# Kernel tuning notes

Measured on AMD Instinct MI355X. Metric: run time of the kernel, lower is better.

Reference implementation:

```python
import math
import jax, jax.numpy as jnp
import numpy as np

N, T, F, H, C, P = 4096, 4, 256, 8, 16, 1024
D = F // H
RECONS_ERROR_LAMBDA = 0.1
L2_LAMBDA = 0.2
RECONS_LAMBDA = 0.01


def _xavier(key, shape):
    fan = shape[-1] + shape[-2]
    lim = math.sqrt(6.0 / fan)
    return jax.random.uniform(key, shape, minval=-lim, maxval=lim, dtype=jnp.float32)


def setup_inputs() -> dict:
    k = jax.random.split(jax.random.key(0), 12)
    return {
        "feature": jax.random.normal(k[0], (N, F), dtype=jnp.float32),
        "mask": (jax.random.uniform(k[1], (N, T, 1, N)) < 0.5).astype(jnp.float32),
        "node_multi_mask": jax.random.randint(k[2], (N,), 0, T),
        "node_idx": jax.random.randint(k[3], (P,), 0, N),
        "theta_w": _xavier(k[4], (F, F)),
        "theta_b": jnp.zeros((F,), jnp.float32),
        "linear": _xavier(k[5], (N, T, 1, N)),
        "recon_proj": _xavier(k[6], (T * T, F, F)),
        "mh_node_proj": _xavier(k[7], (T, F, F)),
        "mh_edge_proj": _xavier(k[8], (T * T, F, F)),
        "pred_w": _xavier(k[9], (C, F)),
        "pred_b": jnp.zeros((C,), jnp.float32),
    }


def reference(feature, mask, node_multi_mask, node_idx, theta_w, theta_b,
              linear, recon_proj, mh_node_proj, mh_edge_proj, pred_w, pred_b):
    nmm = node_multi_mask
    rows = jnp.arange(N)

    # theta linear
    feature = feature @ theta_w.T + theta_b  # [N,F]
    ff = jax.lax.stop_gradient(feature)      # feature.detach()

    # ---- HHEdgeCons ----
    linear_mask = linear * mask                              # [N,T,1,N]
    linear_selected = jnp.where(linear_mask > 0, linear_mask, 0.0)
    ls = linear_selected[:, :, 0, :]                         # [N,T,N]
    # matmul(linear_selected, inp_4_recon).squeeze(): each type t sees the same ff
    reconstruct = jnp.einsum('ntm,mf->ntf', ls, ff)          # [N,T,F]
    # node_project: out[i,j] = recon_proj[nmm[i]*T + j] @ ff[i]
    rp = recon_proj.reshape(T, T, F, F)
    proj_all = jnp.einsum('sjfg,ig->sijf', rp, ff)           # [T,N,T,F]
    inp_proj = proj_all[nmm, rows]                           # [N,T,F]
    l1 = jnp.sum(jnp.abs(ls))
    l2 = jnp.sum(jnp.sqrt(jnp.sum(ls * ls, axis=-1)))
    diff = inp_proj - reconstruct
    recon_error = jnp.sum(jnp.sqrt(jnp.sum(diff * diff, axis=-1)))
    recon_loss = RECONS_ERROR_LAMBDA * (RECONS_LAMBDA * recon_error + L2_LAMBDA * l2 + l1)

    # ---- HHEdgeMP ----
    edge_fea = jnp.einsum('ntm,mf->ntf', ls, feature) + feature[:, None, :]  # [N,T,F]
    edge_norm = jnp.sum(ls, axis=-1) + 1.0                   # [N,T]
    edge_fea = edge_fea / edge_norm[..., None]

    # ---- MultiheadWeight ----
    node_all = jnp.einsum('sfg,ng->snf', mh_node_proj, feature)  # [T,N,F]
    node_projd = node_all[nmm, rows]                             # [N,F]
    ep = mh_edge_proj.reshape(T, T, F, F)
    edge_all = jnp.einsum('sjfg,njg->snjf', ep, edge_fea)        # [T,N,T,F]
    edge_projd = edge_all[nmm, rows]                             # [N,T,F]
    node_multi = node_projd.reshape(N, 1, H, D).transpose(0, 2, 1, 3) / math.sqrt(D)  # [N,H,1,D]
    edge_multi = edge_projd.reshape(N, T, H, D).transpose(0, 2, 3, 1)                 # [N,H,D,T]
    scores = node_multi @ edge_multi                             # [N,H,1,T]
    # nn.Softmax(dim=1) -> over head axis
    all_r_weight = jax.nn.softmax(scores, axis=1).transpose(0, 3, 1, 2)  # [N,T,H,1]

    # ---- HHNodeMP (dropout = identity in eval) ----
    edge_mp = edge_fea.reshape(N, T, H, D)
    weighted = (all_r_weight * edge_mp).reshape(N, T, F)
    node_rep = jnp.sum(jax.nn.relu(weighted), axis=1)            # [N,F]

    # ---- Predictor (dropout = identity) ----
    logits = node_rep[node_idx] @ pred_w.T + pred_b              # [P,C]
    predict = jax.nn.softmax(jax.nn.sigmoid(logits), axis=1)
    return predict, recon_loss, node_rep
```

## Files before the change

kernel.cpp:

```cpp
#include <hip/hip_runtime.h>
#include <hip/hip_bf16.h>
#include <math.h>

#define NN 4096
#define NTROWS 16384

typedef __attribute__((ext_vector_type(8))) __bf16 bf16x8;
typedef __attribute__((ext_vector_type(4))) float f32x4;

static constexpr size_t OFF_SCAL   = 0;
static constexpr size_t OFF_CNT    = 64;
static constexpr size_t OFF_BASE   = 80;
static constexpr size_t OFF_PERM   = 256;
static constexpr size_t OFF_FEAT32 = 16896;
static constexpr size_t OFF_FEATB  = 4211200;
static constexpr size_t OFF_FEATPK = 6308352;
static constexpr size_t OFF_PACKS  = 8405504;
static constexpr size_t OFF_R      = 13255168;
static constexpr size_t OFF_EF32   = 30032384;
static constexpr size_t OFF_EFB    = 46809600;
static constexpr size_t OFF_NPROJ  = 55198208;
static constexpr size_t OFF_EPROJ  = 59392512;

__device__ __forceinline__ f32x4 mm_bf16(bf16x8 a, bf16x8 b, f32x4 c){
  return __builtin_amdgcn_mfma_f32_16x16x32_bf16(a, b, c, 0, 0, 0);
}

__global__ __launch_bounds__(256) void k1b_pack(
    const float* __restrict__ theta, const float* __restrict__ recp,
    const float* __restrict__ nodp,  const float* __restrict__ edgp,
    __bf16* __restrict__ packs)
{
  int b = blockIdx.x;
  const float* src;
  if (b == 0)       src = theta;
  else if (b < 17)  src = recp + (size_t)(b-1)*65536;
  else if (b < 21)  src = nodp + (size_t)(b-17)*65536;
  else              src = edgp + (size_t)(b-21)*65536;
  __bf16* dst = packs + (size_t)b*65536;
  for (int it = 0; it < 32; ++it){
    int u = it*256 + threadIdx.x;
    int lane = u & 63, cf = (u>>6)&15, ks = u>>10;
    int lo = lane & 15, hi = lane >> 4;
    const float* sp = src + (size_t)(cf*16+lo)*256 + ks*32 + hi*8;
    f32x4 a = *(const f32x4*)sp;
    f32x4 c = *(const f32x4*)(sp + 4);
    bf16x8 v;
    v[0]=(__bf16)a[0]; v[1]=(__bf16)a[1]; v[2]=(__bf16)a[2]; v[3]=(__bf16)a[3];
    v[4]=(__bf16)c[0]; v[5]=(__bf16)c[1]; v[6]=(__bf16)c[2]; v[7]=(__bf16)c[3];
    *(bf16x8*)(dst + (size_t)u*8) = v;
  }
}

__global__ __launch_bounds__(256) void k1c_pack(
    const float* __restrict__ feat32, __bf16* __restrict__ featPK)
{
  int u = blockIdx.x*256 + threadIdx.x;
  int lane = u & 63, cf = (u>>6)&15, ks = u>>10;
  int lo = lane & 15, hi = lane >> 4;
  const float* sp = feat32 + (size_t)(ks*32 + hi*8)*256 + cf*16 + lo;
  bf16x8 v;
#pragma unroll
  for (int i = 0; i < 8; ++i) v[i] = (__bf16)sp[(size_t)i*256];
  *(bf16x8*)(featPK + (size_t)u*8) = v;
}

__global__ __launch_bounds__(1024) void kbucket(
    const int* __restrict__ nmm, int* __restrict__ perm,
    int* __restrict__ counts, int* __restrict__ baseo)
{
  __shared__ int cl[4], bl[4], cur[4];
  int t = threadIdx.x;
  if (t < 4) cl[t] = 0;
  __syncthreads();
  for (int i = t; i < NN; i += 1024) atomicAdd(&cl[nmm[i]], 1);
  __syncthreads();
  if (t == 0){ int b = 0; for (int s = 0; s < 4; ++s){ bl[s] = b; b += cl[s]; } }
  __syncthreads();
  if (t < 4){ counts[t] = cl[t]; baseo[t] = bl[t]; cur[t] = bl[t]; }
  __syncthreads();
  for (int i = t; i < NN; i += 1024){
    int s = nmm[i];
    int p = atomicAdd(&cur[s], 1);
    perm[p] = i;
  }
}

template<int MODE>
__global__ __launch_bounds__(256) void gk(
    const __bf16* __restrict__ packs,
    const float*  __restrict__ featureA,
    const __bf16* __restrict__ featBA,
    const __bf16* __restrict__ efBA,
    const float*  __restrict__ tb,
    const float*  __restrict__ Rb,
    float* __restrict__ feat32o, __bf16* __restrict__ featBo,
    float* __restrict__ nprojo,  float* __restrict__ eprojo,
    float* __restrict__ scal,
    const int* __restrict__ perm, const int* __restrict__ counts,
    const int* __restrict__ baseo)
{
  __shared__ __align__(16) __bf16 Al[64*264];
  __shared__ int gidx[64];
  __shared__ float rowsq[64];
  const int t = threadIdx.x, lane = t & 63, wv = t >> 6;
  const int tile = blockIdx.x, combo = blockIdx.y;
  int s = 0, j = 0, cnt;
  const __bf16* B;
  const int rbase = tile * 64;
  if constexpr (MODE == 0){
    cnt = NN; B = packs;
  } else {
    if constexpr (MODE == 1){ s = combo; } else { s = combo >> 2; j = combo & 3; }
    cnt = counts[s];
    if (rbase >= cnt) return;
    int matb;
    if constexpr (MODE == 1)      matb = 17 + combo;
    else if constexpr (MODE == 2) matb = 1  + combo;
    else                          matb = 21 + combo;
    B = packs + (size_t)matb * 65536;
  }
  {
    int r = t >> 2, seg = t & 3;
    int g;
    if constexpr (MODE == 0) g = rbase + r;
    else { int pos = rbase + r; g = (pos < cnt) ? perm[baseo[s] + pos] : -1; }
    if (seg == 0) gidx[r] = g;
    if (t < 64) rowsq[t] = 0.f;
    __bf16* dstrow = &Al[r*264 + seg*64];
    if constexpr (MODE == 0){
      const float* srcp = featureA + (size_t)g*256 + seg*64;
#pragma unroll
      for (int q = 0; q < 8; ++q){
        f32x4 a = *(const f32x4*)(srcp + q*8);
        f32x4 c = *(const f32x4*)(srcp + q*8 + 4);
        bf16x8 v;
        v[0]=(__bf16)a[0]; v[1]=(__bf16)a[1]; v[2]=(__bf16)a[2]; v[3]=(__bf16)a[3];
        v[4]=(__bf16)c[0]; v[5]=(__bf16)c[1]; v[6]=(__bf16)c[2]; v[7]=(__bf16)c[3];
        *(bf16x8*)(dstrow + q*8) = v;
      }
    } else {
      const __bf16* srcp;
      if constexpr (MODE == 3) srcp = efBA + ((size_t)g*4 + j)*256 + seg*64;
      else                     srcp = featBA + (size_t)g*256 + seg*64;
      bf16x8 z;
#pragma unroll
      for (int i = 0; i < 8; ++i) z[i] = (__bf16)0.f;
#pragma unroll
      for (int q = 0; q < 8; ++q){
        bf16x8 v = (g >= 0) ? *(const bf16x8*)(srcp + q*8) : z;
        *(bf16x8*)(dstrow + q*8) = v;
      }
    }
  }
  __syncthreads();
  f32x4 acc[4][4];
#pragma unroll
  for (int a1 = 0; a1 < 4; ++a1)
#pragma unroll
    for (int a2 = 0; a2 < 4; ++a2){ f32x4 z = {0.f,0.f,0.f,0.f}; acc[a1][a2] = z; }
  const int m = lane & 15, h = lane >> 4;
#pragma unroll
  for (int ks = 0; ks < 8; ++ks){
    bf16x8 a[4];
#pragma unroll
    for (int rf = 0; rf < 4; ++rf)
      a[rf] = *(const bf16x8*)&Al[(rf*16 + m)*264 + ks*32 + h*8];
#pragma unroll
    for (int c4 = 0; c4 < 4; ++c4){
      int cf = wv*4 + c4;
      bf16x8 b = *(const bf16x8*)(B + ((size_t)(ks*16 + cf)*64 + lane)*8);
#pragma unroll
      for (int rf = 0; rf < 4; ++rf) acc[rf][c4] = mm_bf16(a[rf], b, acc[rf][c4]);
    }
  }
  if constexpr (MODE == 2){
#pragma unroll
    for (int rf = 0; rf < 4; ++rf)
#pragma unroll
      for (int reg = 0; reg < 4; ++reg){
        int row_l = rf*16 + h*4 + reg;
        int g2 = gidx[row_l];
        float sum = 0.f;
        if (g2 >= 0){
#pragma unroll
          for (int c4 = 0; c4 < 4; ++c4){
            int f = (wv*4 + c4)*16 + m;
            float d = acc[rf][c4][reg] - Rb[((size_t)g2*4 + j)*256 + f];
            sum += d*d;
          }
        }
        sum += __shfl_xor(sum, 1); sum += __shfl_xor(sum, 2);
        sum += __shfl_xor(sum, 4); sum += __shfl_xor(sum, 8);
        if (m == 0) atomicAdd(&rowsq[row_l], sum);
      }
    __syncthreads();
    if (t < 64){
      float e = sqrtf(rowsq[t]);
      e += __shfl_xor(e, 1);  e += __shfl_xor(e, 2);  e += __shfl_xor(e, 4);
      e += __shfl_xor(e, 8);  e += __shfl_xor(e, 16); e += __shfl_xor(e, 32);
      if (t == 0) atomicAdd(&scal[2], e);
    }
  } else {
#pragma unroll
    for (int rf = 0; rf < 4; ++rf)
#pragma unroll
      for (int c4 = 0; c4 < 4; ++c4){
        int f = (wv*4 + c4)*16 + m;
#pragma unroll
        for (int reg = 0; reg < 4; ++reg){
          int row_l = rf*16 + h*4 + reg;
          float val = acc[rf][c4][reg];
          if constexpr (MODE == 0){
            int n = rbase + row_l;
            float v2 = val + tb[f];
            feat32o[(size_t)n*256 + f] = v2;
            featBo[(size_t)n*256 + f] = (__bf16)v2;
          } else {
            int g2 = gidx[row_l];
            if (g2 >= 0){
              if constexpr (MODE == 1) nprojo[(size_t)g2*256 + f] = val;
              else eprojo[((size_t)g2*4 + j)*256 + f] = val;
            }
          }
        }
      }
  }
}

__global__ __launch_bounds__(512) void k2_main(
    const float* __restrict__ linear, const float* __restrict__ maskp,
    const __bf16* __restrict__ featPK, const float* __restrict__ feat32,
    float* __restrict__ Rb, float* __restrict__ ef32, __bf16* __restrict__ efB,
    float* __restrict__ scal)
{
  __shared__ __align__(16) __bf16 Al[64*72];
  __shared__ float ninv[64];
  const int t = threadIdx.x, lane = t & 63, wv = t >> 6;
  const int R0 = blockIdx.x * 64;
  const int r = t >> 3, ko = (t & 7) * 8;
  const float* lp = linear + (size_t)(R0 + r)*4096 + ko;
  const float* mp = maskp  + (size_t)(R0 + r)*4096 + ko;
  f32x4 l0 = *(const f32x4*)lp, l1r = *(const f32x4*)(lp + 4);
  f32x4 m0 = *(const f32x4*)mp, m1r = *(const f32x4*)(mp + 4);
  float rs = 0.f, rq = 0.f;
  f32x4 acc[4][2];
#pragma unroll
  for (int a1 = 0; a1 < 4; ++a1)
#pragma unroll
    for (int a2 = 0; a2 < 2; ++a2){ f32x4 z = {0.f,0.f,0.f,0.f}; acc[a1][a2] = z; }
  const int m = lane & 15, h = lane >> 4;

  for (int kc = 0; kc < 64; ++kc){
    __syncthreads();
    float v[8];
    v[0]=l0[0]*m0[0]; v[1]=l0[1]*m0[1]; v[2]=l0[2]*m0[2]; v[3]=l0[3]*m0[3];
    v[4]=l1r[0]*m1r[0]; v[5]=l1r[1]*m1r[1]; v[6]=l1r[2]*m1r[2]; v[7]=l1r[3]*m1r[3];
    bf16x8 pk;
#pragma unroll
    for (int i = 0; i < 8; ++i){
      float x = v[i] > 0.f ? v[i] : 0.f;
      rs += x; rq += x*x;
      pk[i] = (__bf16)x;
    }
    *(bf16x8*)&Al[r*72 + ko] = pk;
    if (kc < 63){
      lp += 64; mp += 64;
      l0 = *(const f32x4*)lp; l1r = *(const f32x4*)(lp + 4);
      m0 = *(const f32x4*)mp; m1r = *(const f32x4*)(mp + 4);
    }
    __syncthreads();
#pragma unroll
    for (int kl = 0; kl < 2; ++kl){
      bf16x8 a[4];
#pragma unroll
      for (int rf = 0; rf < 4; ++rf)
        a[rf] = *(const bf16x8*)&Al[(rf*16 + m)*72 + kl*32 + h*8];
#pragma unroll
      for (int ci = 0; ci < 2; ++ci){
        int cf = wv*2 + ci;
        bf16x8 b = *(const bf16x8*)(featPK + ((size_t)((kc*2 + kl)*16 + cf)*64 + lane)*8);
#pragma unroll
        for (int rf = 0; rf < 4; ++rf) acc[rf][ci] = mm_bf16(a[rf], b, acc[rf][ci]);
      }
    }
  }
  rs += __shfl_xor(rs, 1); rs += __shfl_xor(rs, 2); rs += __shfl_xor(rs, 4);
  rq += __shfl_xor(rq, 1); rq += __shfl_xor(rq, 2); rq += __shfl_xor(rq, 4);
  if ((t & 7) == 0) ninv[r] = 1.f/(rs + 1.f);
  float c1 = ((t & 7) == 0) ? rs : 0.f;
  float c2 = ((t & 7) == 0) ? sqrtf(rq) : 0.f;
#pragma unroll
  for (int msk = 1; msk < 64; msk <<= 1){
    c1 += __shfl_xor(c1, msk); c2 += __shfl_xor(c2, msk);
  }
  if (lane == 0){ atomicAdd(&scal[0], c1); atomicAdd(&scal[1], c2); }
  __syncthreads();
#pragma unroll
  for (int rf = 0; rf < 4; ++rf)
#pragma unroll
    for (int ci = 0; ci < 2; ++ci){
      int f = (wv*2 + ci)*16 + m;
#pragma unroll
      for (int reg = 0; reg < 4; ++reg){
        int row_l = rf*16 + h*4 + reg;
        float val = acc[rf][ci][reg];
        size_t gi = (size_t)(R0 + row_l)*256 + f;
        Rb[gi] = val;
        int n = (R0 + row_l) >> 2;
        float e = (val + feat32[(size_t)n*256 + f]) * ninv[row_l];
        ef32[gi] = e;
        efB[gi] = (__bf16)e;
      }
    }
}

__global__ __launch_bounds__(256) void k6_attn(
    const float* __restrict__ nproj, const float* __restrict__ eproj,
    const float* __restrict__ ef32, float* __restrict__ nrep)
{
  const int i = blockIdx.x, f = threadIdx.x, hh = f >> 5;
  __shared__ float sc[4][8];
  float np = nproj[(size_t)i*256 + f] * 0.17677669529663689f;
#pragma unroll
  for (int t4 = 0; t4 < 4; ++t4){
    float p = np * eproj[((size_t)i*4 + t4)*256 + f];
    p += __shfl_xor(p, 16); p += __shfl_xor(p, 8); p += __shfl_xor(p, 4);
    p += __shfl_xor(p, 2);  p += __shfl_xor(p, 1);
    if ((f & 31) == 0) sc[t4][hh] = p;
  }
  __syncthreads();
  float accv = 0.f;
#pragma unroll
  for (int t4 = 0; t4 < 4; ++t4){
    float mx = sc[t4][0];
#pragma unroll
    for (int q = 1; q < 8; ++q) mx = fmaxf(mx, sc[t4][q]);
    float den = 0.f;
#pragma unroll
    for (int q = 0; q < 8; ++q) den += expf(sc[t4][q] - mx);
    float w = expf(sc[t4][hh] - mx) / den;
    float x = w * ef32[((size_t)i*4 + t4)*256 + f];
    accv += x > 0.f ? x : 0.f;
  }
  nrep[(size_t)i*256 + f] = accv;
}

__global__ void k_loss(const float* __restrict__ scal, float* __restrict__ o){
  if (threadIdx.x == 0 && blockIdx.x == 0)
    o[0] = 0.1f*(0.01f*scal[2] + 0.2f*scal[1] + scal[0]);
}

__global__ __launch_bounds__(256) void k7_pred(
    const float* __restrict__ nrep, const int* __restrict__ nidx,
    const float* __restrict__ pw, const float* __restrict__ pb,
    float* __restrict__ outp)
{
  __shared__ float pwT[256*16];
  const int t = threadIdx.x;
  {
    int c0 = t & 15, k0 = (t >> 4) * 16;
    for (int kk = 0; kk < 16; ++kk)
      pwT[(k0 + kk)*16 + c0] = pw[(size_t)c0*256 + k0 + kk];
  }
  __syncthreads();
  const int c = t & 15, r0 = t >> 4;
  float pbv = pb[c];
  for (int rr = 0; rr < 4; ++rr){
    int p = blockIdx.x*64 + rr*16 + r0;
    int i = nidx[p];
    const float* nr = nrep + (size_t)i*256;
    float acc = pbv;
    for (int k = 0; k < 256; ++k) acc += nr[k]*pwT[k*16 + c];
    float sg = 1.f/(1.f + expf(-acc));
    float mx = sg;
    mx = fmaxf(mx, __shfl_xor(mx, 1)); mx = fmaxf(mx, __shfl_xor(mx, 2));
    mx = fmaxf(mx, __shfl_xor(mx, 4)); mx = fmaxf(mx, __shfl_xor(mx, 8));
    float ex = expf(sg - mx);
    float den = ex;
    den += __shfl_xor(den, 1); den += __shfl_xor(den, 2);
    den += __shfl_xor(den, 4); den += __shfl_xor(den, 8);
    outp[(size_t)p*16 + c] = ex/den;
  }
}

extern "C" void kernel_launch(void* const* d_in, const int* in_sizes, int n_in,
                              void* d_out, int out_size, void* d_ws, size_t ws_size,
                              hipStream_t stream)
{
  (void)in_sizes; (void)n_in; (void)out_size; (void)ws_size;
  const float* feature = (const float*)d_in[0];
  const float* maskp   = (const float*)d_in[1];
  const int*   nmm     = (const int*)d_in[2];
  const int*   nidx    = (const int*)d_in[3];
  const float* theta_w = (const float*)d_in[4];
  const float* theta_b = (const float*)d_in[5];
  const float* linear  = (const float*)d_in[6];
  const float* recon_p = (const float*)d_in[7];
  const float* node_p  = (const float*)d_in[8];
  const float* edge_p  = (const float*)d_in[9];
  const float* pred_w  = (const float*)d_in[10];
  const float* pred_b  = (const float*)d_in[11];
  float* out = (float*)d_out;
  char* ws = (char*)d_ws;

  float* scal   = (float*)(ws + OFF_SCAL);
  int*   counts = (int*)(ws + OFF_CNT);
  int*   baseo  = (int*)(ws + OFF_BASE);
  int*   perm   = (int*)(ws + OFF_PERM);
  float* feat32 = (float*)(ws + OFF_FEAT32);
  __bf16* featB  = (__bf16*)(ws + OFF_FEATB);
  __bf16* featPK = (__bf16*)(ws + OFF_FEATPK);
  __bf16* packs  = (__bf16*)(ws + OFF_PACKS);
  float* Rbuf   = (float*)(ws + OFF_R);
  float* ef32   = (float*)(ws + OFF_EF32);
  __bf16* efB    = (__bf16*)(ws + OFF_EFB);
  float* nproj  = (float*)(ws + OFF_NPROJ);
  float* eproj  = (float*)(ws + OFF_EPROJ);

  float* out_pred = out;
  float* out_loss = out + 16384;
  float* out_nrep = out + 16385;

  hipMemsetAsync(d_ws, 0, 96, stream);

  k1b_pack<<<37, 256, 0, stream>>>(theta_w, recon_p, node_p, edge_p, packs);

  gk<0><<<dim3(64, 1), 256, 0, stream>>>(packs, feature, nullptr, nullptr, theta_b,
      nullptr, feat32, featB, nullptr, nullptr, scal, perm, counts, baseo);

  k1c_pack<<<512, 256, 0, stream>>>(feat32, featPK);

  kbucket<<<1, 1024, 0, stream>>>(nmm, perm, counts, baseo);

  k2_main<<<256, 512, 0, stream>>>(linear, maskp, featPK, feat32,
                                   Rbuf, ef32, efB, scal);

  gk<2><<<dim3(64, 16), 256, 0, stream>>>(packs, nullptr, featB, nullptr, nullptr,
      Rbuf, nullptr, nullptr, nullptr, nullptr, scal, perm, counts, baseo);

  gk<3><<<dim3(64, 16), 256, 0, stream>>>(packs, nullptr, featB, efB, nullptr,
      nullptr, nullptr, nullptr, nullptr, eproj, scal, perm, counts, baseo);

  gk<1><<<dim3(64, 4), 256, 0, stream>>>(packs, nullptr, featB, nullptr, nullptr,
      nullptr, nullptr, nullptr, nproj, nullptr, scal, perm, counts, baseo);

  k6_attn<<<4096, 256, 0, stream>>>(nproj, eproj, ef32, out_nrep);

  k_loss<<<1, 64, 0, stream>>>(scal, out_loss);

  k7_pred<<<16, 256, 0, stream>>>(out_nrep, nidx, pred_w, pred_b, out_pred);
}
```

Measured before the change: 847.1 us.

## Split-K the masked reconstruction GEMM and merge projection GEMMs into one launch

The main masked-linear GEMM (k2_main) now splits its K=4096 reduction across 4 blocks per row tile, using a double-buffered LDS tile. Partial results are accumulated with atomics into a zeroed R buffer, and per-row sum and sum-of-squares are also accumulated with atomics. A new k2b kernel then does the normalization, builds the edge features and reduces the losses. The three projection GEMM launches are fused into a single gk_all grid. kbucket is rewritten to use wave ballots instead of shared atomics and is launched first. The aim is to fill more CUs with the memory-bound 256-block GEMM and cut launch count, at the cost of a 17MB memset, float atomics (nondeterministic summation order) and an extra pass over R.

```diff
diff --git a/kernel.cpp b/kernel.cpp
--- a/kernel.cpp
+++ b/kernel.cpp
@@ -17,10 +17,12 @@
 static constexpr size_t OFF_FEATPK = 6308352;
 static constexpr size_t OFF_PACKS  = 8405504;
 static constexpr size_t OFF_R      = 13255168;
-static constexpr size_t OFF_EF32   = 30032384;
-static constexpr size_t OFF_EFB    = 46809600;
-static constexpr size_t OFF_NPROJ  = 55198208;
-static constexpr size_t OFF_EPROJ  = 59392512;
+static constexpr size_t OFF_RSUM   = 30032384;
+static constexpr size_t OFF_RSQ    = 30097920;
+static constexpr size_t OFF_EF32   = 30163456;
+static constexpr size_t OFF_EFB    = 46940672;
+static constexpr size_t OFF_NPROJ  = 55329280;
+static constexpr size_t OFF_EPROJ  = 59523584;
 
 __device__ __forceinline__ f32x4 mm_bf16(bf16x8 a, bf16x8 b, f32x4 c){
   return __builtin_amdgcn_mfma_f32_16x16x32_bf16(a, b, c, 0, 0, 0);
@@ -69,88 +71,70 @@
     const int* __restrict__ nmm, int* __restrict__ perm,
     int* __restrict__ counts, int* __restrict__ baseo)
 {
-  __shared__ int cl[4], bl[4], cur[4];
-  int t = threadIdx.x;
-  if (t < 4) cl[t] = 0;
-  __syncthreads();
-  for (int i = t; i < NN; i += 1024) atomicAdd(&cl[nmm[i]], 1);
-  __syncthreads();
-  if (t == 0){ int b = 0; for (int s = 0; s < 4; ++s){ bl[s] = b; b += cl[s]; } }
-  __syncthreads();
-  if (t < 4){ counts[t] = cl[t]; baseo[t] = bl[t]; cur[t] = bl[t]; }
-  __syncthreads();
-  for (int i = t; i < NN; i += 1024){
+  __shared__ int segoff[64][4];
+  __shared__ int bl[4];
+  const int t = threadIdx.x, lane = t & 63, w = t >> 6;
+  int sv[4];
+#pragma unroll
+  for (int it = 0; it < 4; ++it){
+    int i = it*1024 + t;
     int s = nmm[i];
-    int p = atomicAdd(&cur[s], 1);
-    perm[p] = i;
-  }
-}
-
-template<int MODE>
-__global__ __launch_bounds__(256) void gk(
-    const __bf16* __restrict__ packs,
-    const float*  __restrict__ featureA,
-    const __bf16* __restrict__ featBA,
-    const __bf16* __restrict__ efBA,
-    const float*  __restrict__ tb,
-    const float*  __restrict__ Rb,
-    float* __restrict__ feat32o, __bf16* __restrict__ featBo,
-    float* __restrict__ nprojo,  float* __restrict__ eprojo,
-    float* __restrict__ scal,
-    const int* __restrict__ perm, const int* __restrict__ counts,
-    const int* __restrict__ baseo)
+    sv[it] = s;
+#pragma unroll
+    for (int b = 0; b < 4; ++b){
+      unsigned long long mb = __ballot(s == b);
+      if (lane == 0) segoff[it*16 + w][b] = __popcll(mb);
+    }
+  }
+  __syncthreads();
+  if (t < 4){
+    int b = t, run = 0;
+    for (int seg = 0; seg < 64; ++seg){
+      int c = segoff[seg][b]; segoff[seg][b] = run; run += c;
+    }
+    counts[b] = run;
+  }
+  __syncthreads();
+  if (t == 0){
+    int b0 = 0;
+    for (int s = 0; s < 4; ++s){ bl[s] = b0; baseo[s] = b0; b0 += counts[s]; }
+  }
+  __syncthreads();
+#pragma unroll
+  for (int it = 0; it < 4; ++it){
+    int i = it*1024 + t;
+    int s = sv[it];
+    int rank = 0;
+#pragma unroll
+    for (int b = 0; b < 4; ++b){
+      unsigned long long mb = __ballot(s == b);
+      if (s == b) rank = __popcll(mb & ((1ull << lane) - 1ull));
+    }
+    perm[bl[s] + segoff[it*16 + w][s] + rank] = i;
+  }
+}
+
+__global__ __launch_bounds__(256) void k0_feat(
+    const __bf16* __restrict__ packs, const float* __restrict__ featureA,
+    const float* __restrict__ tb,
+    float* __restrict__ feat32o, __bf16* __restrict__ featBo)
 {
   __shared__ __align__(16) __bf16 Al[64*264];
-  __shared__ int gidx[64];
-  __shared__ float rowsq[64];
   const int t = threadIdx.x, lane = t & 63, wv = t >> 6;
-  const int tile = blockIdx.x, combo = blockIdx.y;
-  int s = 0, j = 0, cnt;
-  const __bf16* B;
-  const int rbase = tile * 64;
-  if constexpr (MODE == 0){
-    cnt = NN; B = packs;
-  } else {
-    if constexpr (MODE == 1){ s = combo; } else { s = combo >> 2; j = combo & 3; }
-    cnt = counts[s];
-    if (rbase >= cnt) return;
-    int matb;
-    if constexpr (MODE == 1)      matb = 17 + combo;
-    else if constexpr (MODE == 2) matb = 1  + combo;
-    else                          matb = 21 + combo;
-    B = packs + (size_t)matb * 65536;
-  }
+  const int rbase = blockIdx.x * 64;
+  const __bf16* B = packs;
   {
     int r = t >> 2, seg = t & 3;
-    int g;
-    if constexpr (MODE == 0) g = rbase + r;
-    else { int pos = rbase + r; g = (pos < cnt) ? perm[baseo[s] + pos] : -1; }
-    if (seg == 0) gidx[r] = g;
-    if (t < 64) rowsq[t] = 0.f;
+    const float* srcp = featureA + (size_t)(rbase + r)*256 + seg*64;
     __bf16* dstrow = &Al[r*264 + seg*64];
-    if constexpr (MODE == 0){
-      const float* srcp = featureA + (size_t)g*256 + seg*64;
-#pragma unroll
-      for (int q = 0; q < 8; ++q){
-        f32x4 a = *(const f32x4*)(srcp + q*8);
-        f32x4 c = *(const f32x4*)(srcp + q*8 + 4);
-        bf16x8 v;
-        v[0]=(__bf16)a[0]; v[1]=(__bf16)a[1]; v[2]=(__bf16)a[2]; v[3]=(__bf16)a[3];
-        v[4]=(__bf16)c[0]; v[5]=(__bf16)c[1]; v[6]=(__bf16)c[2]; v[7]=(__bf16)c[3];
-        *(bf16x8*)(dstrow + q*8) = v;
-      }
-    } else {
-      const __bf16* srcp;
-      if constexpr (MODE == 3) srcp = efBA + ((size_t)g*4 + j)*256 + seg*64;
-      else                     srcp = featBA + (size_t)g*256 + seg*64;
-      bf16x8 z;
-#pragma unroll
-      for (int i = 0; i < 8; ++i) z[i] = (__bf16)0.f;
-#pragma unroll
-      for (int q = 0; q < 8; ++q){
-        bf16x8 v = (g >= 0) ? *(const bf16x8*)(srcp + q*8) : z;
-        *(bf16x8*)(dstrow + q*8) = v;
-      }
+#pragma unroll
+    for (int q = 0; q < 8; ++q){
+      f32x4 a = *(const f32x4*)(srcp + q*8);
+      f32x4 c = *(const f32x4*)(srcp + q*8 + 4);
+      bf16x8 v;
+      v[0]=(__bf16)a[0]; v[1]=(__bf16)a[1]; v[2]=(__bf16)a[2]; v[3]=(__bf16)a[3];
+      v[4]=(__bf16)c[0]; v[5]=(__bf16)c[1]; v[6]=(__bf16)c[2]; v[7]=(__bf16)c[3];
+      *(bf16x8*)(dstrow + q*8) = v;
     }
   }
   __syncthreads();
@@ -174,7 +158,184 @@
       for (int rf = 0; rf < 4; ++rf) acc[rf][c4] = mm_bf16(a[rf], b, acc[rf][c4]);
     }
   }
-  if constexpr (MODE == 2){
+#pragma unroll
+  for (int rf = 0; rf < 4; ++rf)
+#pragma unroll
+    for (int c4 = 0; c4 < 4; ++c4){
+      int f = (wv*4 + c4)*16 + m;
+#pragma unroll
+      for (int reg = 0; reg < 4; ++reg){
+        int n = rbase + rf*16 + h*4 + reg;
+        float v2 = acc[rf][c4][reg] + tb[f];
+        feat32o[(size_t)n*256 + f] = v2;
+        featBo[(size_t)n*256 + f] = (__bf16)v2;
+      }
+    }
+}
+
+__global__ __launch_bounds__(512, 4) void k2_main(
+    const float* __restrict__ linear, const float* __restrict__ maskp,
+    const __bf16* __restrict__ featPK,
+    float* __restrict__ Rb, float* __restrict__ rowsum, float* __restrict__ rowsq)
+{
+  __shared__ __align__(16) __bf16 Al[2][64*72];
+  const int t = threadIdx.x, lane = t & 63, wv = t >> 6;
+  const int R0 = blockIdx.x * 64;
+  const int ksl = blockIdx.y;
+  const int r = t >> 3, ko = (t & 7) * 8;
+  const float* lp = linear + (size_t)(R0 + r)*4096 + ksl*1024 + ko;
+  const float* mp = maskp  + (size_t)(R0 + r)*4096 + ksl*1024 + ko;
+  const __bf16* Bp = featPK + (((size_t)(ksl*32)*16 + wv*2)*64 + lane)*8;
+  f32x4 l0 = *(const f32x4*)lp, l1r = *(const f32x4*)(lp + 4);
+  f32x4 m0 = *(const f32x4*)mp, m1r = *(const f32x4*)(mp + 4);
+  float rs = 0.f, rq = 0.f;
+  f32x4 acc[4][2];
+#pragma unroll
+  for (int a1 = 0; a1 < 4; ++a1)
+#pragma unroll
+    for (int a2 = 0; a2 < 2; ++a2){ f32x4 z = {0.f,0.f,0.f,0.f}; acc[a1][a2] = z; }
+  const int m = lane & 15, h = lane >> 4;
+
+  for (int kc = 0; kc < 16; ++kc){
+    bf16x8 b[2][2];
+#pragma unroll
+    for (int kl = 0; kl < 2; ++kl)
+#pragma unroll
+      for (int ci = 0; ci < 2; ++ci)
+        b[kl][ci] = *(const bf16x8*)(Bp + (size_t)(kc*2 + kl)*8192 + ci*512);
+    __builtin_amdgcn_sched_barrier(0);
+    float v[8];
+    v[0]=l0[0]*m0[0]; v[1]=l0[1]*m0[1]; v[2]=l0[2]*m0[2]; v[3]=l0[3]*m0[3];
+    v[4]=l1r[0]*m1r[0]; v[5]=l1r[1]*m1r[1]; v[6]=l1r[2]*m1r[2]; v[7]=l1r[3]*m1r[3];
+    bf16x8 pk;
+#pragma unroll
+    for (int i = 0; i < 8; ++i){
+      float x = v[i] > 0.f ? v[i] : 0.f;
+      rs += x; rq += x*x;
+      pk[i] = (__bf16)x;
+    }
+    *(bf16x8*)&Al[kc & 1][r*72 + ko] = pk;
+    if (kc < 15){
+      lp += 64; mp += 64;
+      l0 = *(const f32x4*)lp; l1r = *(const f32x4*)(lp + 4);
+      m0 = *(const f32x4*)mp; m1r = *(const f32x4*)(mp + 4);
+    }
+    __builtin_amdgcn_sched_barrier(0);
+    __syncthreads();
+#pragma unroll
+    for (int kl = 0; kl < 2; ++kl){
+      bf16x8 a[4];
+#pragma unroll
+      for (int rf = 0; rf < 4; ++rf)
+        a[rf] = *(const bf16x8*)&Al[kc & 1][(rf*16 + m)*72 + kl*32 + h*8];
+#pragma unroll
+      for (int ci = 0; ci < 2; ++ci)
+#pragma unroll
+        for (int rf = 0; rf < 4; ++rf) acc[rf][ci] = mm_bf16(a[rf], b[kl][ci], acc[rf][ci]);
+    }
+  }
+  rs += __shfl_xor(rs, 1); rs += __shfl_xor(rs, 2); rs += __shfl_xor(rs, 4);
+  rq += __shfl_xor(rq, 1); rq += __shfl_xor(rq, 2); rq += __shfl_xor(rq, 4);
+  if ((t & 7) == 0){
+    atomicAdd(&rowsum[R0 + r], rs);
+    atomicAdd(&rowsq[R0 + r], rq);
+  }
+#pragma unroll
+  for (int rf = 0; rf < 4; ++rf)
+#pragma unroll
+    for (int ci = 0; ci < 2; ++ci){
+      int f = (wv*2 + ci)*16 + m;
+#pragma unroll
+      for (int reg = 0; reg < 4; ++reg){
+        int row_l = rf*16 + h*4 + reg;
+        atomicAdd(&Rb[(size_t)(R0 + row_l)*256 + f], acc[rf][ci][reg]);
+      }
+    }
+}
+
+__global__ __launch_bounds__(256) void k2b(
+    const float* __restrict__ Rb, const float* __restrict__ feat32,
+    const float* __restrict__ rowsum, const float* __restrict__ rowsq,
+    float* __restrict__ ef32, __bf16* __restrict__ efB, float* __restrict__ scal)
+{
+  const int t = threadIdx.x;
+  const int row0 = blockIdx.x * 16;
+#pragma unroll 4
+  for (int rr = 0; rr < 16; ++rr){
+    int row = row0 + rr, n = row >> 2;
+    float ninv = 1.f / (rowsum[row] + 1.f);
+    size_t gi = (size_t)row*256 + t;
+    float e = (Rb[gi] + feat32[(size_t)n*256 + t]) * ninv;
+    ef32[gi] = e;
+    efB[gi] = (__bf16)e;
+  }
+  float c1 = 0.f, c2 = 0.f;
+  if (t < 16){ int row = row0 + t; c1 = rowsum[row]; c2 = sqrtf(rowsq[row]); }
+  c1 += __shfl_xor(c1, 1); c1 += __shfl_xor(c1, 2); c1 += __shfl_xor(c1, 4); c1 += __shfl_xor(c1, 8);
+  c2 += __shfl_xor(c2, 1); c2 += __shfl_xor(c2, 2); c2 += __shfl_xor(c2, 4); c2 += __shfl_xor(c2, 8);
+  if (t == 0){ atomicAdd(&scal[0], c1); atomicAdd(&scal[1], c2); }
+}
+
+__global__ __launch_bounds__(256) void gk_all(
+    const __bf16* __restrict__ packs, const __bf16* __restrict__ featB,
+    const __bf16* __restrict__ efB, const float* __restrict__ Rb,
+    float* __restrict__ nproj, float* __restrict__ eproj, float* __restrict__ scal,
+    const int* __restrict__ perm, const int* __restrict__ counts,
+    const int* __restrict__ baseo)
+{
+  __shared__ __align__(16) __bf16 Al[64*264];
+  __shared__ int gidx[64];
+  __shared__ float rowsq_l[64];
+  const int t = threadIdx.x, lane = t & 63, wv = t >> 6;
+  const int y = blockIdx.y;
+  int mode, s, j, matb;
+  if (y < 16){ mode = 2; s = y >> 2; j = y & 3; matb = 1 + y; }
+  else if (y < 32){ int y2 = y - 16; mode = 3; s = y2 >> 2; j = y2 & 3; matb = 21 + y2; }
+  else { mode = 1; s = y - 32; j = 0; matb = 17 + s; }
+  const int cnt = counts[s];
+  const int rbase = blockIdx.x * 64;
+  if (rbase >= cnt) return;
+  const __bf16* B = packs + (size_t)matb * 65536;
+  {
+    int r = t >> 2, seg = t & 3;
+    int pos = rbase + r;
+    int g = (pos < cnt) ? perm[baseo[s] + pos] : -1;
+    if (seg == 0) gidx[r] = g;
+    if (t < 64) rowsq_l[t] = 0.f;
+    const __bf16* srcp = (mode == 3) ? efB + ((size_t)g*4 + j)*256 + seg*64
+                                     : featB + (size_t)g*256 + seg*64;
+    __bf16* dstrow = &Al[r*264 + seg*64];
+    bf16x8 z;
+#pragma unroll
+    for (int i = 0; i < 8; ++i) z[i] = (__bf16)0.f;
+#pragma unroll
+    for (int q = 0; q < 8; ++q){
+      bf16x8 v = (g >= 0) ? *(const bf16x8*)(srcp + q*8) : z;
+      *(bf16x8*)(dstrow + q*8) = v;
+    }
+  }
+  __syncthreads();
+  f32x4 acc[4][4];
+#pragma unroll
+  for (int a1 = 0; a1 < 4; ++a1)
+#pragma unroll
+    for (int a2 = 0; a2 < 4; ++a2){ f32x4 z = {0.f,0.f,0.f,0.f}; acc[a1][a2] = z; }
+  const int m = lane & 15, h = lane >> 4;
+#pragma unroll
+  for (int ks = 0; ks < 8; ++ks){
+    bf16x8 a[4];
+#pragma unroll
+    for (int rf = 0; rf < 4; ++rf)
+      a[rf] = *(const bf16x8*)&Al[(rf*16 + m)*264 + ks*32 + h*8];
+#pragma unroll
+    for (int c4 = 0; c4 < 4; ++c4){
+      int cf = wv*4 + c4;
+      bf16x8 b = *(const bf16x8*)(B + ((size_t)(ks*16 + cf)*64 + lane)*8);
+#pragma unroll
+      for (int rf = 0; rf < 4; ++rf) acc[rf][c4] = mm_bf16(a[rf], b, acc[rf][c4]);
+    }
+  }
+  if (mode == 2){
 #pragma unroll
     for (int rf = 0; rf < 4; ++rf)
 #pragma unroll
@@ -192,11 +353,11 @@
         }
         sum += __shfl_xor(sum, 1); sum += __shfl_xor(sum, 2);
         sum += __shfl_xor(sum, 4); sum += __shfl_xor(sum, 8);
-        if (m == 0) atomicAdd(&rowsq[row_l], sum);
+        if (m == 0) atomicAdd(&rowsq_l[row_l], sum);
       }
     __syncthreads();
     if (t < 64){
-      float e = sqrtf(rowsq[t]);
+      float e = sqrtf(rowsq_l[t]);
       e += __shfl_xor(e, 1);  e += __shfl_xor(e, 2);  e += __shfl_xor(e, 4);
       e += __shfl_xor(e, 8);  e += __shfl_xor(e, 16); e += __shfl_xor(e, 32);
       if (t == 0) atomicAdd(&scal[2], e);
@@ -210,109 +371,14 @@
 #pragma unroll
         for (int reg = 0; reg < 4; ++reg){
           int row_l = rf*16 + h*4 + reg;
-          float val = acc[rf][c4][reg];
-          if constexpr (MODE == 0){
-            int n = rbase + row_l;
-            float v2 = val + tb[f];
-            feat32o[(size_t)n*256 + f] = v2;
-            featBo[(size_t)n*256 + f] = (__bf16)v2;
-          } else {
-            int g2 = gidx[row_l];
-            if (g2 >= 0){
-              if constexpr (MODE == 1) nprojo[(size_t)g2*256 + f] = val;
-              else eprojo[((size_t)g2*4 + j)*256 + f] = val;
-            }
+          int g2 = gidx[row_l];
+          if (g2 >= 0){
+            if (mode == 1) nproj[(size_t)g2*256 + f] = acc[rf][c4][reg];
+            else           eproj[((size_t)g2*4 + j)*256 + f] = acc[rf][c4][reg];
           }
         }
       }
   }
-}
-
-__global__ __launch_bounds__(512) void k2_main(
-    const float* __restrict__ linear, const float* __restrict__ maskp,
-    const __bf16* __restrict__ featPK, const float* __restrict__ feat32,
-    float* __restrict__ Rb, float* __restrict__ ef32, __bf16* __restrict__ efB,
-    float* __restrict__ scal)
-{
-  __shared__ __align__(16) __bf16 Al[64*72];
-  __shared__ float ninv[64];
-  const int t = threadIdx.x, lane = t & 63, wv = t >> 6;
-  const int R0 = blockIdx.x * 64;
-  const int r = t >> 3, ko = (t & 7) * 8;
-  const float* lp = linear + (size_t)(R0 + r)*4096 + ko;
-  const float* mp = maskp  + (size_t)(R0 + r)*4096 + ko;
-  f32x4 l0 = *(const f32x4*)lp, l1r = *(const f32x4*)(lp + 4);
-  f32x4 m0 = *(const f32x4*)mp, m1r = *(const f32x4*)(mp + 4);
-  float rs = 0.f, rq = 0.f;
-  f32x4 acc[4][2];
-#pragma unroll
-  for (int a1 = 0; a1 < 4; ++a1)
-#pragma unroll
-    for (int a2 = 0; a2 < 2; ++a2){ f32x4 z = {0.f,0.f,0.f,0.f}; acc[a1][a2] = z; }
-  const int m = lane & 15, h = lane >> 4;
-
-  for (int kc = 0; kc < 64; ++kc){
-    __syncthreads();
-    float v[8];
-    v[0]=l0[0]*m0[0]; v[1]=l0[1]*m0[1]; v[2]=l0[2]*m0[2]; v[3]=l0[3]*m0[3];
-    v[4]=l1r[0]*m1r[0]; v[5]=l1r[1]*m1r[1]; v[6]=l1r[2]*m1r[2]; v[7]=l1r[3]*m1r[3];
-    bf16x8 pk;
-#pragma unroll
-    for (int i = 0; i < 8; ++i){
-      float x = v[i] > 0.f ? v[i] : 0.f;
-      rs += x; rq += x*x;
-      pk[i] = (__bf16)x;
-    }
-    *(bf16x8*)&Al[r*72 + ko] = pk;
-    if (kc < 63){
-      lp += 64; mp += 64;
-      l0 = *(const f32x4*)lp; l1r = *(const f32x4*)(lp + 4);
-      m0 = *(const f32x4*)mp; m1r = *(const f32x4*)(mp + 4);
-    }
-    __syncthreads();
-#pragma unroll
-    for (int kl = 0; kl < 2; ++kl){
-      bf16x8 a[4];
-#pragma unroll
-      for (int rf = 0; rf < 4; ++rf)
-        a[rf] = *(const bf16x8*)&Al[(rf*16 + m)*72 + kl*32 + h*8];
-#pragma unroll
-      for (int ci = 0; ci < 2; ++ci){
-        int cf = wv*2 + ci;
-        bf16x8 b = *(const bf16x8*)(featPK + ((size_t)((kc*2 + kl)*16 + cf)*64 + lane)*8);
-#pragma unroll
-        for (int rf = 0; rf < 4; ++rf) acc[rf][ci] = mm_bf16(a[rf], b, acc[rf][ci]);
-      }
-    }
-  }
-  rs += __shfl_xor(rs, 1); rs += __shfl_xor(rs, 2); rs += __shfl_xor(rs, 4);
-  rq += __shfl_xor(rq, 1); rq += __shfl_xor(rq, 2); rq += __shfl_xor(rq, 4);
-  if ((t & 7) == 0) ninv[r] = 1.f/(rs + 1.f);
-  float c1 = ((t & 7) == 0) ? rs : 0.f;
-  float c2 = ((t & 7) == 0) ? sqrtf(rq) : 0.f;
-#pragma unroll
-  for (int msk = 1; msk < 64; msk <<= 1){
-    c1 += __shfl_xor(c1, msk); c2 += __shfl_xor(c2, msk);
-  }
-  if (lane == 0){ atomicAdd(&scal[0], c1); atomicAdd(&scal[1], c2); }
-  __syncthreads();
-#pragma unroll
-  for (int rf = 0; rf < 4; ++rf)
-#pragma unroll
-    for (int ci = 0; ci < 2; ++ci){
-      int f = (wv*2 + ci)*16 + m;
-#pragma unroll
-      for (int reg = 0; reg < 4; ++reg){
-        int row_l = rf*16 + h*4 + reg;
-        float val = acc[rf][ci][reg];
-        size_t gi = (size_t)(R0 + row_l)*256 + f;
-        Rb[gi] = val;
-        int n = (R0 + row_l) >> 2;
-        float e = (val + feat32[(size_t)n*256 + f]) * ninv[row_l];
-        ef32[gi] = e;
-        efB[gi] = (__bf16)e;
-      }
-    }
 }
 
 __global__ __launch_bounds__(256) void k6_attn(
@@ -413,6 +479,8 @@
   __bf16* featPK = (__bf16*)(ws + OFF_FEATPK);
   __bf16* packs  = (__bf16*)(ws + OFF_PACKS);
   float* Rbuf   = (float*)(ws + OFF_R);
+  float* rowsum = (float*)(ws + OFF_RSUM);
+  float* rowsq  = (float*)(ws + OFF_RSQ);
   float* ef32   = (float*)(ws + OFF_EF32);
   __bf16* efB    = (__bf16*)(ws + OFF_EFB);
   float* nproj  = (float*)(ws + OFF_NPROJ);
@@ -422,28 +490,24 @@
   float* out_loss = out + 16384;
   float* out_nrep = out + 16385;
 
-  hipMemsetAsync(d_ws, 0, 96, stream);
+  hipMemsetAsync(ws + OFF_SCAL, 0, 96, stream);
+  hipMemsetAsync(ws + OFF_R, 0, 16777216 + 131072, stream);
+
+  kbucket<<<1, 1024, 0, stream>>>(nmm, perm, counts, baseo);
 
   k1b_pack<<<37, 256, 0, stream>>>(theta_w, recon_p, node_p, edge_p, packs);
 
-  gk<0><<<dim3(64, 1), 256, 0, stream>>>(packs, feature, nullptr, nullptr, theta_b,
-      nullptr, feat32, featB, nullptr, nullptr, scal, perm, counts, baseo);
+  k0_feat<<<64, 256, 0, stream>>>(packs, feature, theta_b, feat32, featB);
 
   k1c_pack<<<512, 256, 0, stream>>>(feat32, featPK);
 
-  kbucket<<<1, 1024, 0, stream>>>(nmm, perm, counts, baseo);
-
-  k2_main<<<256, 512, 0, stream>>>(linear, maskp, featPK, feat32,
-                                   Rbuf, ef32, efB, scal);
-
-  gk<2><<<dim3(64, 16), 256, 0, stream>>>(packs, nullptr, featB, nullptr, nullptr,
-      Rbuf, nullptr, nullptr, nullptr, nullptr, scal, perm, counts, baseo);
-
-  gk<3><<<dim3(64, 16), 256, 0, stream>>>(packs, nullptr, featB, efB, nullptr,
-      nullptr, nullptr, nullptr, nullptr, eproj, scal, perm, counts, baseo);
-
-  gk<1><<<dim3(64, 4), 256, 0, stream>>>(packs, nullptr, featB, nullptr, nullptr,
-      nullptr, nullptr, nullptr, nproj, nullptr, scal, perm, counts, baseo);
+  k2_main<<<dim3(256, 4), 512, 0, stream>>>(linear, maskp, featPK,
+                                            Rbuf, rowsum, rowsq);
+
+  k2b<<<1024, 256, 0, stream>>>(Rbuf, feat32, rowsum, rowsq, ef32, efB, scal);
+
+  gk_all<<<dim3(64, 36), 256, 0, stream>>>(packs, featB, efB, Rbuf,
+      nproj, eproj, scal, perm, counts, baseo);
 
   k6_attn<<<4096, 256, 0, stream>>>(nproj, eproj, ef32, out_nrep);
 
```

Result: faster. 725.7 us (-14.3%).
